# Performance work log

Hardware: AMD Instinct MI355X
Metric: run time of the kernel (lower is better)

Reference implementation:

```python
import jax, jax.numpy as jnp
import numpy as np

B, D_IN, UNITS = 2048, 4096, 4096

def setup_inputs() -> dict:
    key = jax.random.key(0)
    k_x, k_m, k_w, k_b = jax.random.split(key, 4)
    x = jax.random.normal(k_x, (B, D_IN), dtype=jnp.float32)
    mask = jax.random.randint(k_m, (D_IN, UNITS), 0, 2).astype(jnp.float32)
    # glorot_uniform kernel
    limit = np.sqrt(6.0 / (D_IN + UNITS)).astype(np.float32)
    W = jax.random.uniform(k_w, (D_IN, UNITS), dtype=jnp.float32, minval=-limit, maxval=limit)
    b = jnp.zeros((UNITS,), dtype=jnp.float32)
    return {"x": x, "mask": mask, "W": W, "b": b}

def reference(x, mask, W, b):
    # Original: build COO sparse tensor of kernel entries where mask != 0,
    # then (sparse_W^T @ x^T)^T == x @ (W masked by mask != 0). Bias added, no activation.
    W_masked = jnp.where(mask != 0.0, W, jnp.zeros((), dtype=W.dtype))
    return x @ W_masked + b
```

## Files before the change

kernel.cpp:

```cpp
#include <hip/hip_runtime.h>

#define M_DIM 2048
#define K_DIM 4096
#define N_DIM 4096

typedef unsigned short u16;
typedef __bf16 bf16x8 __attribute__((ext_vector_type(8)));
typedef float f32x4 __attribute__((ext_vector_type(4)));
typedef u16 u16x4 __attribute__((ext_vector_type(4)));
typedef u16 u16x8 __attribute__((ext_vector_type(8)));

__device__ __forceinline__ u16 f2bf(float f) {
    unsigned int u = __float_as_uint(f);
    u += 0x7fffu + ((u >> 16) & 1u);
    return (u16)(u >> 16);
}

__device__ __forceinline__ void load16(const void* g, void* l) {
    __builtin_amdgcn_global_load_lds(
        (__attribute__((address_space(1))) const void*)g,
        (__attribute__((address_space(3))) void*)l,
        16, 0, 0);
}

__global__ __launch_bounds__(256) void conv_x(const float* __restrict__ x,
                                              u16* __restrict__ xb) {
    size_t i = ((size_t)blockIdx.x * 256 + threadIdx.x) * 4;
    float4 v = *(const float4*)(x + i);
    u16x4 o;
    o.x = f2bf(v.x); o.y = f2bf(v.y); o.z = f2bf(v.z); o.w = f2bf(v.w);
    *(u16x4*)(xb + i) = o;
}

__global__ __launch_bounds__(256) void mask_transpose(const float* __restrict__ W,
                                                      const float* __restrict__ Msk,
                                                      u16* __restrict__ Bt) {
    __shared__ __align__(16) u16 T[64][68];
    const int n0 = blockIdx.x * 64;
    const int k0 = blockIdx.y * 64;
    const int t  = threadIdx.x;

    const int colq = (t & 15) * 4;
    const int row4 = t >> 4;
#pragma unroll
    for (int p = 0; p < 4; ++p) {
        int row = row4 + p * 16;
        size_t g = (size_t)(k0 + row) * N_DIM + n0 + colq;
        float4 w = *(const float4*)(W + g);
        float4 m = *(const float4*)(Msk + g);
        u16x4 v;
        v.x = f2bf(m.x != 0.f ? w.x : 0.f);
        v.y = f2bf(m.y != 0.f ? w.y : 0.f);
        v.z = f2bf(m.z != 0.f ? w.z : 0.f);
        v.w = f2bf(m.w != 0.f ? w.w : 0.f);
        *(u16x4*)&T[row][colq] = v;
    }
    __syncthreads();

    const int kc  = (t & 7) * 8;
    const int nr0 = t >> 3;
#pragma unroll
    for (int p = 0; p < 2; ++p) {
        int nr = nr0 + p * 32;
        u16x8 v;
#pragma unroll
        for (int i = 0; i < 8; ++i) v[i] = T[kc + i][nr];
        *(u16x8*)(Bt + (size_t)(n0 + nr) * K_DIM + k0 + kc) = v;
    }
}

__global__ __launch_bounds__(256) void gemm_bt(const u16* __restrict__ A,
                                               const u16* __restrict__ Bt,
                                               const float* __restrict__ bias,
                                               float* __restrict__ C) {
    __shared__ __align__(16) u16 As[128 * 64];
    __shared__ __align__(16) u16 Bs[128 * 64];

    const int t  = threadIdx.x;
    const int bn = blockIdx.x;
    const int bm = blockIdx.y;

    const u16* gA = A  + (size_t)(bm * 128 + (t >> 3)) * K_DIM + (t & 7) * 8;
    const u16* gB = Bt + (size_t)(bn * 128 + (t >> 3)) * K_DIM + (t & 7) * 8;
    u16* lA = As + (t >> 3) * 64 + (t & 7) * 8;
    u16* lB = Bs + (t >> 3) * 64 + (t & 7) * 8;

    const int lane = t & 63;
    const int wave = t >> 6;
    const int wm = (wave >> 1) * 64;
    const int wn = (wave & 1) * 64;
    const int fr = lane & 15;
    const int fk = (lane >> 4) * 8;

    f32x4 acc[4][4] = {};

    for (int k0 = 0; k0 < K_DIM; k0 += 64) {
#pragma unroll
        for (int it = 0; it < 4; ++it) {
            load16(gA + k0 + it * 32 * K_DIM, lA + it * 32 * 64);
            load16(gB + k0 + it * 32 * K_DIM, lB + it * 32 * 64);
        }
        __syncthreads();
#pragma unroll
        for (int kk = 0; kk < 64; kk += 32) {
            bf16x8 af[4], bf[4];
#pragma unroll
            for (int i = 0; i < 4; ++i)
                af[i] = *(const bf16x8*)(As + (wm + i * 16 + fr) * 64 + kk + fk);
#pragma unroll
            for (int j = 0; j < 4; ++j)
                bf[j] = *(const bf16x8*)(Bs + (wn + j * 16 + fr) * 64 + kk + fk);
#pragma unroll
            for (int i = 0; i < 4; ++i)
#pragma unroll
                for (int j = 0; j < 4; ++j)
                    acc[i][j] = __builtin_amdgcn_mfma_f32_16x16x32_bf16(
                        af[i], bf[j], acc[i][j], 0, 0, 0);
        }
        __syncthreads();
    }

    const int rb = (lane >> 4) * 4;
#pragma unroll
    for (int i = 0; i < 4; ++i) {
#pragma unroll
        for (int j = 0; j < 4; ++j) {
            int n = bn * 128 + wn + j * 16 + fr;
            float bv = bias[n];
#pragma unroll
            for (int r = 0; r < 4; ++r) {
                int m = bm * 128 + wm + i * 16 + rb + r;
                C[(size_t)m * N_DIM + n] = acc[i][j][r] + bv;
            }
        }
    }
}

extern "C" void kernel_launch(void* const* d_in, const int* in_sizes, int n_in,
                              void* d_out, int out_size, void* d_ws, size_t ws_size,
                              hipStream_t stream) {
    const float* x    = (const float*)d_in[0];
    const float* mask = (const float*)d_in[1];
    const float* W    = (const float*)d_in[2];
    const float* bias = (const float*)d_in[3];
    float* out = (float*)d_out;

    u16* Bt = (u16*)d_ws;
    u16* xb = (u16*)d_ws + (size_t)N_DIM * K_DIM;

    conv_x<<<(M_DIM * K_DIM) / (256 * 4), 256, 0, stream>>>(x, xb);
    mask_transpose<<<dim3(N_DIM / 64, K_DIM / 64), 256, 0, stream>>>(W, mask, Bt);
    gemm_bt<<<dim3(N_DIM / 128, M_DIM / 128), 256, 0, stream>>>(xb, Bt, bias, out);
}
```

Measured before the change: 280.9 us.

## Swizzle GEMM LDS tiles via XOR and merge prep kernels into one launch

The two preprocessing kernels (x conversion to bf16 and masked W transpose) are merged into a single launch, with block index selecting the role and each conversion thread handling 8 elements. The GEMM now writes global-to-LDS loads in an XOR-swizzled layout: each thread fetches the global chunk (t&7)^(row&7), and the MFMA fragment reads use the matching swizzled columns. This is meant to remove LDS bank conflicts on the 16-byte fragment reads and to save one kernel launch. It adds index arithmetic, and correctness depends on the swizzle matching on both the store and load sides.

```diff
diff --git a/kernel.cpp b/kernel.cpp
--- a/kernel.cpp
+++ b/kernel.cpp
@@ -23,22 +23,25 @@
         16, 0, 0);
 }
 
-__global__ __launch_bounds__(256) void conv_x(const float* __restrict__ x,
-                                              u16* __restrict__ xb) {
-    size_t i = ((size_t)blockIdx.x * 256 + threadIdx.x) * 4;
-    float4 v = *(const float4*)(x + i);
-    u16x4 o;
-    o.x = f2bf(v.x); o.y = f2bf(v.y); o.z = f2bf(v.z); o.w = f2bf(v.w);
-    *(u16x4*)(xb + i) = o;
-}
-
-__global__ __launch_bounds__(256) void mask_transpose(const float* __restrict__ W,
-                                                      const float* __restrict__ Msk,
-                                                      u16* __restrict__ Bt) {
+__global__ __launch_bounds__(256) void prep(const float* __restrict__ x,
+                                            u16* __restrict__ xb,
+                                            const float* __restrict__ W,
+                                            const float* __restrict__ Msk,
+                                            u16* __restrict__ Bt) {
+    const int t = threadIdx.x;
+    if (blockIdx.x >= 4096) {
+        size_t i = ((size_t)(blockIdx.x - 4096) * 256 + t) * 8;
+        float4 v0 = *(const float4*)(x + i);
+        float4 v1 = *(const float4*)(x + i + 4);
+        u16x8 o;
+        o[0] = f2bf(v0.x); o[1] = f2bf(v0.y); o[2] = f2bf(v0.z); o[3] = f2bf(v0.w);
+        o[4] = f2bf(v1.x); o[5] = f2bf(v1.y); o[6] = f2bf(v1.z); o[7] = f2bf(v1.w);
+        *(u16x8*)(xb + i) = o;
+        return;
+    }
     __shared__ __align__(16) u16 T[64][68];
-    const int n0 = blockIdx.x * 64;
-    const int k0 = blockIdx.y * 64;
-    const int t  = threadIdx.x;
+    const int n0 = (blockIdx.x & 63) * 64;
+    const int k0 = (blockIdx.x >> 6) * 64;
 
     const int colq = (t & 15) * 4;
     const int row4 = t >> 4;
@@ -80,47 +83,53 @@
     const int bn = blockIdx.x;
     const int bm = blockIdx.y;
 
-    const u16* gA = A  + (size_t)(bm * 128 + (t >> 3)) * K_DIM + (t & 7) * 8;
-    const u16* gB = Bt + (size_t)(bn * 128 + (t >> 3)) * K_DIM + (t & 7) * 8;
-    u16* lA = As + (t >> 3) * 64 + (t & 7) * 8;
-    u16* lB = Bs + (t >> 3) * 64 + (t & 7) * 8;
+    const int srow   = t >> 3;
+    const int schunk = (t & 7) ^ (srow & 7);
+    const u16* gA = A  + (size_t)(bm * 128 + srow) * K_DIM + schunk * 8;
+    const u16* gB = Bt + (size_t)(bn * 128 + srow) * K_DIM + schunk * 8;
+    u16* lA = As + t * 8;
+    u16* lB = Bs + t * 8;
 
     const int lane = t & 63;
     const int wave = t >> 6;
     const int wm = (wave >> 1) * 64;
     const int wn = (wave & 1) * 64;
     const int fr = lane & 15;
-    const int fk = (lane >> 4) * 8;
+    const int q  = lane >> 4;
+    const int sw = fr & 7;
+    const int col0 = ((0 + q) ^ sw) * 8;
+    const int col1 = ((4 + q) ^ sw) * 8;
 
     f32x4 acc[4][4] = {};
 
     for (int k0 = 0; k0 < K_DIM; k0 += 64) {
 #pragma unroll
         for (int it = 0; it < 4; ++it) {
-            load16(gA + k0 + it * 32 * K_DIM, lA + it * 32 * 64);
-            load16(gB + k0 + it * 32 * K_DIM, lB + it * 32 * 64);
+            load16(gA + k0 + it * 32 * K_DIM, lA + it * 2048);
+            load16(gB + k0 + it * 32 * K_DIM, lB + it * 2048);
         }
         __syncthreads();
 #pragma unroll
-        for (int kk = 0; kk < 64; kk += 32) {
-            bf16x8 af[4], bf[4];
+        for (int kx = 0; kx < 2; ++kx) {
+            const int col = kx ? col1 : col0;
+            bf16x8 af[4], bfr[4];
 #pragma unroll
             for (int i = 0; i < 4; ++i)
-                af[i] = *(const bf16x8*)(As + (wm + i * 16 + fr) * 64 + kk + fk);
+                af[i] = *(const bf16x8*)(As + (wm + i * 16 + fr) * 64 + col);
 #pragma unroll
             for (int j = 0; j < 4; ++j)
-                bf[j] = *(const bf16x8*)(Bs + (wn + j * 16 + fr) * 64 + kk + fk);
+                bfr[j] = *(const bf16x8*)(Bs + (wn + j * 16 + fr) * 64 + col);
 #pragma unroll
             for (int i = 0; i < 4; ++i)
 #pragma unroll
                 for (int j = 0; j < 4; ++j)
                     acc[i][j] = __builtin_amdgcn_mfma_f32_16x16x32_bf16(
-                        af[i], bf[j], acc[i][j], 0, 0, 0);
+                        af[i], bfr[j], acc[i][j], 0, 0, 0);
         }
         __syncthreads();
     }
 
-    const int rb = (lane >> 4) * 4;
+    const int rb = q * 4;
 #pragma unroll
     for (int i = 0; i < 4; ++i) {
 #pragma unroll
@@ -148,7 +157,6 @@
     u16* Bt = (u16*)d_ws;
     u16* xb = (u16*)d_ws + (size_t)N_DIM * K_DIM;
 
-    conv_x<<<(M_DIM * K_DIM) / (256 * 4), 256, 0, stream>>>(x, xb);
-    mask_transpose<<<dim3(N_DIM / 64, K_DIM / 64), 256, 0, stream>>>(W, mask, Bt);
+    prep<<<8192, 256, 0, stream>>>(x, xb, W, mask, Bt);
     gemm_bt<<<dim3(N_DIM / 128, M_DIM / 128), 256, 0, stream>>>(xb, Bt, bias, out);
 }
```

Measured after the change: 253.4 us. -9.8%, faster.
